# Kernel optimization log

Hardware: AMD Instinct MI355X
Metric: run time of the kernel (lower is better)

Reference implementation:

```python
import jax, jax.numpy as jnp
from jax import lax
import numpy as np

EPS = 1e-5
DN = ('NCHW', 'OIHW', 'NCHW')


def conv_s2(x, w):
    # Conv2d k=4 s=2 p=1, no bias
    return lax.conv_general_dilated(x, w, (2, 2), [(1, 1), (1, 1)], dimension_numbers=DN)


def deconv_s2(x, w):
    # ConvTranspose2d k=4 s=2 p=1; torch weight layout (in, out, kH, kW)
    w_ = jnp.flip(w, (2, 3)).transpose(1, 0, 2, 3)  # -> (out, in, kH, kW)
    return lax.conv_general_dilated(x, w_, (1, 1), [(2, 2), (2, 2)],
                                    lhs_dilation=(2, 2), dimension_numbers=DN)


def bn_train(x, gamma, beta):
    # BatchNorm2d in training mode: batch stats over (N, H, W), biased variance
    m = jnp.mean(x, axis=(0, 2, 3), keepdims=True)
    v = jnp.var(x, axis=(0, 2, 3), keepdims=True)
    g = gamma.reshape(1, -1, 1, 1)
    b = beta.reshape(1, -1, 1, 1)
    return (x - m) * jax.lax.rsqrt(v + EPS) * g + b


def lrelu(x):
    return jnp.where(x >= 0, x, 0.2 * x)


def setup_inputs() -> dict:
    key = jax.random.key(0)
    ks = jax.random.split(key, 32)
    nef = 64
    d = {}
    d['x'] = jax.random.normal(ks[0], (256, 3, 64, 64), dtype=jnp.float32)
    # encoder conv weights (O, I, 4, 4), init N(0, 0.02)
    d['w1'] = 0.02 * jax.random.normal(ks[1], (nef, 3, 4, 4), jnp.float32)
    d['w2'] = 0.02 * jax.random.normal(ks[2], (nef * 2, nef, 4, 4), jnp.float32)
    d['w3'] = 0.02 * jax.random.normal(ks[3], (nef * 4, nef * 2, 4, 4), jnp.float32)
    d['w4'] = 0.02 * jax.random.normal(ks[4], (nef * 8, nef * 4, 4, 4), jnp.float32)
    # bn params: weight ~ N(1, 0.02), bias = 0
    for i, c in enumerate([nef, nef * 2, nef * 4, nef * 8]):
        d[f'g{i+1}'] = 1.0 + 0.02 * jax.random.normal(ks[5 + i], (c,), jnp.float32)
        d[f'b{i+1}'] = jnp.zeros((c,), jnp.float32)
    # 512 channel-wise Linear(16,16): torch default init U(-1/4, 1/4)
    bound = 1.0 / 4.0
    d['cw_w'] = jax.random.uniform(ks[9], (512, 16, 16), jnp.float32, -bound, bound)
    d['cw_b'] = jax.random.uniform(ks[10], (512, 16), jnp.float32, -bound, bound)
    # decoder deconv weights in torch layout (in, out, 4, 4)
    d['dw1'] = 0.02 * jax.random.normal(ks[11], (nef * 8, nef * 4, 4, 4), jnp.float32)
    d['dw2'] = 0.02 * jax.random.normal(ks[12], (nef * 4, nef * 2, 4, 4), jnp.float32)
    d['dw3'] = 0.02 * jax.random.normal(ks[13], (nef * 2, nef, 4, 4), jnp.float32)
    d['dw4'] = 0.02 * jax.random.normal(ks[14], (nef, 3, 4, 4), jnp.float32)
    for i, c in enumerate([nef * 4, nef * 2, nef]):
        d[f'dg{i+1}'] = 1.0 + 0.02 * jax.random.normal(ks[15 + i], (c,), jnp.float32)
        d[f'db{i+1}'] = jnp.zeros((c,), jnp.float32)
    return d


def reference(x, w1, w2, w3, w4, g1, b1, g2, b2, g3, b3, g4, b4,
              cw_w, cw_b, dw1, dw2, dw3, dw4, dg1, db1, dg2, db2, dg3, db3):
    h = lrelu(bn_train(conv_s2(x, w1), g1, b1))
    h = lrelu(bn_train(conv_s2(h, w2), g2, b2))
    h = lrelu(bn_train(conv_s2(h, w3), g3, b3))
    h = lrelu(bn_train(conv_s2(h, w4), g4, b4))  # (B, 512, 4, 4)
    B, C, H, W = h.shape
    flat = h.reshape(B, C, H * W)  # (B, 512, 16)
    # per-channel Linear: y[b,c,t] = sum_s flat[b,c,s] * cw_w[c,t,s] + cw_b[c,t]
    flat = jnp.einsum('bcs,cts->bct', flat, cw_w) + cw_b[None, :, :]
    h = flat.reshape(B, C, H, W)
    h = jax.nn.relu(bn_train(deconv_s2(h, dw1), dg1, db1))
    h = jax.nn.relu(bn_train(deconv_s2(h, dw2), dg2, db2))
    h = jax.nn.relu(bn_train(deconv_s2(h, dw3), dg3, db3))
    return jnp.tanh(deconv_s2(h, dw4))
```

## Files before the change

kernel.cpp:

```cpp
#include <hip/hip_runtime.h>
#include <math.h>

typedef _Float16 f16;
typedef __attribute__((ext_vector_type(8))) _Float16 f16x8;
typedef __attribute__((ext_vector_type(16))) float f32x16;

union U64x2 { unsigned long long u[2]; f16x8 v; };
union Q16   { uint4 q; unsigned long long u[2]; };

constexpr int ilog2c(int x) { return x <= 1 ? 0 : 1 + ilog2c(x >> 1); }

__device__ __forceinline__ float fast_tanh(float x) {
    float e = __expf(2.f * x);
    return (e - 1.f) / (e + 1.f);
}

__device__ __forceinline__ void barrier_no_vmdrain() {
    asm volatile("s_waitcnt lgkmcnt(0)" ::: "memory");
    __builtin_amdgcn_sched_barrier(0);
    __builtin_amdgcn_s_barrier();
    __builtin_amdgcn_sched_barrier(0);
}

template<int CIN,int IH,int IW,int OH,int OW,int COUT,int COB,int SPT,int KS,
         int CO_FR,bool DEC,bool PAIR>
__global__ __launch_bounds__(256,2) void mfma_conv(
    const f16* __restrict__ xin, const f16* __restrict__ wp,
    f16* __restrict__ out16, float* __restrict__ out32, size_t ps,
    float* __restrict__ psumF, float* __restrict__ psqF)
{
    constexpr int OHo  = DEC ? OH/2 : OH;
    constexpr int OWo  = DEC ? OW/2 : OW;
    constexpr int KTOT = CIN * (DEC ? 4 : 16);
    constexpr int CH   = (KTOT/64) / KS;
    constexpr int RPT  = CIN / 64;
    constexpr int RSH  = (RPT==1?0:RPT==2?1:RPT==4?2:3);
    constexpr int WSTR = CIN * 16;
    constexpr int TPR  = 256 / COB;
    constexpr int SPB  = OHo * OWo;
    constexpr int LSPB = ilog2c(SPB);
    constexpr int LOWo = ilog2c(OWo);

    static_assert(!PAIR || (RPT >= 2 && CH % 2 == 0), "PAIR needs RPT>=2");
    constexpr int CHU  = PAIR ? CH/2 : CH;
    constexpr int RW   = PAIR ? 32 : 16;
    constexpr int PM   = PAIR ? 15 : 7;
    constexpr int KKN  = PAIR ? 8 : 4;
    constexpr int XU4  = PAIR ? 16 : 8;
    constexpr int WSEG = (PAIR ? 128 : 64)/TPR;
    constexpr int WU4  = WSEG / 8;

    __shared__ unsigned long long Xs[SPT*RW];
    __shared__ unsigned long long Wls[COB*RW];

    const int t   = threadIdx.x;
    const int bx  = blockIdx.x;
    const int cob = blockIdx.y;
    const int bz  = blockIdx.z;
    const int par = DEC ? (bz & 3) : 0;
    const int ks  = DEC ? (bz >> 2) : bz;
    const int poh = par >> 1, pw = par & 1;

    const int gsp_s = bx*SPT + t;
    const int img_s = gsp_s >> LSPB;
    const int r_s   = gsp_s & (SPB-1);
    const int oy_s  = r_s >> LOWo;
    const int ox_s  = r_s & (OWo-1);

    const int wco   = t / TPR;
    const int wpart = t % TPR;
    const f16* wbase = wp + (size_t)(cob*COB + wco)*WSTR + wpart*WSEG;

    const int wave = t >> 6, lane = t & 63, half = lane >> 5, l31 = lane & 31;
    const int co_w = (wave >> 1) * (CO_FR*32);
    const int sp_w = (wave & 1) * 128;
    const int swz  = l31 & PM;

    f32x16 acc[CO_FR][4];
    #pragma unroll
    for (int i = 0; i < CO_FR; ++i)
        #pragma unroll
        for (int b = 0; b < 4; ++b)
            #pragma unroll
            for (int r = 0; r < 16; ++r) acc[i][b][r] = 0.f;

    uint4 xreg[XU4];
    uint4 wreg[WU4];

    auto issue = [&](int cc) {
        const int gc  = ks*CH + (PAIR ? 2*cc : cc);
        const int tap = gc >> RSH;
        const int ci0 = (gc & (RPT-1)) << 6;
        int kh, kw, ih, iw;
        if (DEC) {
            const int t2h = tap >> 1, t2w = tap & 1;
            kh = (1-poh) + 2*t2h; kw = (1-pw) + 2*t2w;
            ih = oy_s + poh - t2h; iw = ox_s + pw - t2w;
        } else {
            kh = tap >> 2; kw = tap & 3;
            ih = 2*oy_s - 1 + kh; iw = 2*ox_s - 1 + kw;
        }
        const int woff = (kh*4 + kw)*CIN + ci0;
        const uint4* wsrc = (const uint4*)(wbase + woff);
        #pragma unroll
        for (int j = 0; j < WU4; ++j) wreg[j] = wsrc[j];
        const bool ok = (unsigned)ih < (unsigned)IH && (unsigned)iw < (unsigned)IW;
        if (ok) {
            const uint4* xsrc = (const uint4*)
                (xin + ((size_t)(img_s*IH + ih)*IW + iw)*CIN + ci0);
            #pragma unroll
            for (int j = 0; j < XU4; ++j) xreg[j] = xsrc[j];
        } else {
            #pragma unroll
            for (int j = 0; j < XU4; ++j) xreg[j] = uint4{0u,0u,0u,0u};
        }
    };

    issue(0);

    for (int cc = 0; cc < CHU; ++cc) {
        if (cc) barrier_no_vmdrain();

        #pragma unroll
        for (int j = 0; j < WU4; ++j) {
            Q16 v; v.q = wreg[j];
            const int lp = wpart*WU4 + j;
            const int u0 = wco*RW + ((lp ^ (wco & PM)) << 1);
            Wls[u0]   = v.u[0];
            Wls[u0+1] = v.u[1];
        }
        {
            #pragma unroll
            for (int j = 0; j < XU4; ++j) {
                Q16 v; v.q = xreg[j];
                const int u0 = t*RW + ((j ^ (t & PM)) << 1);
                Xs[u0]   = v.u[0];
                Xs[u0+1] = v.u[1];
            }
        }

        if (cc + 1 < CHU) issue(cc + 1);

        asm volatile("s_waitcnt lgkmcnt(0)" ::: "memory");
        __builtin_amdgcn_sched_barrier(0);
        __builtin_amdgcn_s_barrier();
        __builtin_amdgcn_sched_barrier(0);

        #pragma unroll
        for (int kk = 0; kk < KKN; ++kk) {
            const int so = ((kk*2 + half) ^ swz) << 1;
            f16x8 wf[CO_FR], xf[4];
            #pragma unroll
            for (int i = 0; i < CO_FR; ++i) {
                U64x2 u; const int rw = (co_w + i*32 + l31)*RW + so;
                u.u[0] = Wls[rw]; u.u[1] = Wls[rw+1]; wf[i] = u.v;
            }
            #pragma unroll
            for (int b = 0; b < 4; ++b) {
                U64x2 u; const int rx = (sp_w + b*32 + l31)*RW + so;
                u.u[0] = Xs[rx]; u.u[1] = Xs[rx+1]; xf[b] = u.v;
            }
            #pragma unroll
            for (int i = 0; i < CO_FR; ++i)
                #pragma unroll
                for (int b = 0; b < 4; ++b)
                    acc[i][b] = __builtin_amdgcn_mfma_f32_32x32x16_f16(
                        xf[b], wf[i], acc[i][b], 0, 0, 0);
        }
    }

    #pragma unroll
    for (int b = 0; b < 4; ++b) {
        #pragma unroll
        for (int q = 0; q < 4; ++q) {
            #pragma unroll
            for (int r2 = 0; r2 < 4; ++r2) {
                const int sp_loc = sp_w + b*32 + q*8 + 4*half + r2;
                const int gsp    = bx*SPT + sp_loc;
                size_t base;
                if (DEC) {
                    const int img = gsp >> LSPB;
                    const int r   = gsp & (SPB-1);
                    const int oh  = 2*(r >> LOWo) + poh;
                    const int ow  = 2*(r & (OWo-1)) + pw;
                    base = ((size_t)(img*OH + oh)*OW + ow)*COUT + cob*COB;
                } else {
                    base = (size_t)gsp*COUT + cob*COB;
                }
                #pragma unroll
                for (int i = 0; i < CO_FR; ++i) {
                    const int co_l = co_w + i*32 + l31;
                    const float v  = acc[i][b][q*4 + r2];
                    if (KS == 1) out16[base + co_l] = (_Float16)v;
                    else         out32[(size_t)ks*ps + base + co_l] = v;
                }
            }
        }
    }

    if (KS == 1 && psumF != nullptr) {
        float sArr[CO_FR], qArr[CO_FR];
        #pragma unroll
        for (int i = 0; i < CO_FR; ++i) {
            float s = 0.f, q = 0.f;
            #pragma unroll
            for (int b = 0; b < 4; ++b)
                #pragma unroll
                for (int r = 0; r < 16; ++r) {
                    const float v = acc[i][b][r];
                    s += v; q += v * v;
                }
            s += __shfl_down(s, 32);
            q += __shfl_down(q, 32);
            sArr[i] = s; qArr[i] = q;
        }
        __syncthreads();
        float* LS = (float*)Xs;
        float* LQ = LS + 4*CO_FR*32;
        if (half == 0) {
            #pragma unroll
            for (int i = 0; i < CO_FR; ++i) {
                LS[(wave*CO_FR + i)*32 + l31] = sArr[i];
                LQ[(wave*CO_FR + i)*32 + l31] = qArr[i];
            }
        }
        __syncthreads();
        if (t < COB) {
            constexpr int KSH = (CO_FR == 1 ? 5 : 6);
            const int k  = t >> KSH;
            const int ii = (CO_FR == 1) ? 0 : ((t >> 5) & 1);
            const int l  = t & 31;
            const int i0 = ((2*k)  *CO_FR + ii)*32 + l;
            const int i1 = ((2*k+1)*CO_FR + ii)*32 + l;
            atomicAdd(psumF + cob*COB + t, LS[i0] + LS[i1]);
            atomicAdd(psqF  + cob*COB + t, LQ[i0] + LQ[i1]);
        }
    }
}

__global__ __launch_bounds__(256,2) void conv1_mfma(
    const f16* __restrict__ xp, const f16* __restrict__ wp,
    f16* __restrict__ out, float* __restrict__ psumF, float* __restrict__ psqF)
{
    __shared__ unsigned long long Xs[256*16];
    __shared__ unsigned long long Wls[64*16];
    const int t = threadIdx.x, bx = blockIdx.x;

    {
        const int r = t >> 2, part = t & 3;
        const uint4* src = (const uint4*)(wp + r*64 + part*16);
        Q16 v0; v0.q = src[0];
        Q16 v1; v1.q = src[1];
        const int a0 = r*16 + (((part*2)   ^ (r & 7)) << 1);
        const int a1 = r*16 + (((part*2+1) ^ (r & 7)) << 1);
        Wls[a0]   = v0.u[0]; Wls[a0+1] = v0.u[1];
        Wls[a1]   = v1.u[0]; Wls[a1+1] = v1.u[1];
    }
    {
        const int gsp = bx*256 + t;
        const int n = gsp >> 10, r = gsp & 1023;
        const int oy = r >> 5, ox = r & 31;
        const int ih0 = 2*oy - 1, iw0 = 2*ox - 1;
        #pragma unroll
        for (int tap = 0; tap < 16; ++tap) {
            const int ih = ih0 + (tap >> 2), iw = iw0 + (tap & 3);
            unsigned long long v = 0ull;
            if ((unsigned)ih < 64u && (unsigned)iw < 64u)
                v = *(const unsigned long long*)(xp + (((size_t)n*64 + ih)*64 + iw)*4);
            const int u = t*16 + (((tap >> 1) ^ (t & 7)) << 1) + (tap & 1);
            Xs[u] = v;
        }
    }
    __syncthreads();

    const int wave = t >> 6, lane = t & 63, half = lane >> 5, l31 = lane & 31;
    const int co_w = (wave >> 1) * 32;
    const int sp_w = (wave & 1) * 128;
    const int swz  = l31 & 7;

    f32x16 acc[4];
    #pragma unroll
    for (int b = 0; b < 4; ++b)
        #pragma unroll
        for (int r = 0; r < 16; ++r) acc[b][r] = 0.f;

    #pragma unroll
    for (int kk = 0; kk < 4; ++kk) {
        const int so = ((kk*2 + half) ^ swz) << 1;
        U64x2 uw; const int rw = (co_w + l31)*16 + so;
        uw.u[0] = Wls[rw]; uw.u[1] = Wls[rw+1];
        #pragma unroll
        for (int b = 0; b < 4; ++b) {
            U64x2 ux; const int rx = (sp_w + b*32 + l31)*16 + so;
            ux.u[0] = Xs[rx]; ux.u[1] = Xs[rx+1];
            acc[b] = __builtin_amdgcn_mfma_f32_32x32x16_f16(
                ux.v, uw.v, acc[b], 0, 0, 0);
        }
    }
    #pragma unroll
    for (int b = 0; b < 4; ++b)
        #pragma unroll
        for (int q = 0; q < 4; ++q)
            #pragma unroll
            for (int r2 = 0; r2 < 4; ++r2) {
                const int sp_loc = sp_w + b*32 + q*8 + 4*half + r2;
                out[(size_t)(bx*256 + sp_loc)*64 + co_w + l31] =
                    (_Float16)acc[b][q*4 + r2];
            }

    float s = 0.f, q = 0.f;
    #pragma unroll
    for (int b = 0; b < 4; ++b)
        #pragma unroll
        for (int r = 0; r < 16; ++r) {
            const float v = acc[b][r];
            s += v; q += v * v;
        }
    s += __shfl_down(s, 32);
    q += __shfl_down(q, 32);
    __syncthreads();
    {
        float* LS = (float*)Xs;
        float* LQ = LS + 128;
        if (half == 0) {
            LS[wave*32 + l31] = s;
            LQ[wave*32 + l31] = q;
        }
        __syncthreads();
        if (t < 64) {
            const int k = t >> 5, l = t & 31;
            atomicAdd(psumF + t, LS[(2*k)*32 + l] + LS[(2*k+1)*32 + l]);
            atomicAdd(psqF  + t, LQ[(2*k)*32 + l] + LQ[(2*k+1)*32 + l]);
        }
    }
}

__global__ __launch_bounds__(256,2) void deconv3_pwf(
    const f16* __restrict__ xin, const f16* __restrict__ wp,
    f16* __restrict__ out, float* __restrict__ psumF, float* __restrict__ psqF)
{
    __shared__ unsigned long long Xs[256*16];
    __shared__ unsigned long long Wls[2][64*16];

    const int t   = threadIdx.x;
    const int bx  = blockIdx.x;
    const int poh = blockIdx.y;

    const int gsp_s = bx*256 + t;
    const int img_s = gsp_s >> 8;
    const int r_s   = gsp_s & 255;
    const int oy_s  = r_s >> 4;
    const int ox_s  = r_s & 15;

    const int wco   = t >> 2;
    const int wpart = t & 3;
    const f16* wbase = wp + (size_t)wco*2048 + wpart*16;

    const int wave = t >> 6, lane = t & 63, half = lane >> 5, l31 = lane & 31;
    const int co_w = (wave >> 1) * 32;
    const int sp_w = (wave & 1) * 128;
    const int swz  = l31 & 7;

    f32x16 acc[2][4];
    #pragma unroll
    for (int p = 0; p < 2; ++p)
        #pragma unroll
        for (int b = 0; b < 4; ++b)
            #pragma unroll
            for (int r = 0; r < 16; ++r) acc[p][b][r] = 0.f;

    uint4 xreg[8];
    uint4 wregP[2][2];

    auto issue = [&](int cc) {
        const int seg  = cc & 1;
        const int rest = cc >> 1;
        const int dwi  = rest % 3;
        const int t2h  = rest / 3;
        const int dh = poh - t2h, dw = dwi - 1;
        const int ih = oy_s + dh, iw = ox_s + dw;
        const int ci0 = seg << 6;
        #pragma unroll
        for (int p = 0; p < 2; ++p) {
            const int t2w = p - dw;
            if (t2w == 0 || t2w == 1) {
                const int kh = (1-poh) + 2*t2h, kw = (1-p) + 2*t2w;
                const uint4* wsrc = (const uint4*)(wbase + (kh*4 + kw)*128 + ci0);
                wregP[p][0] = wsrc[0];
                wregP[p][1] = wsrc[1];
            }
        }
        const bool ok = (unsigned)ih < 16u && (unsigned)iw < 16u;
        if (ok) {
            const uint4* xsrc = (const uint4*)
                (xin + ((size_t)(img_s*16 + ih)*16 + iw)*128 + ci0);
            #pragma unroll
            for (int j = 0; j < 8; ++j) xreg[j] = xsrc[j];
        } else {
            #pragma unroll
            for (int j = 0; j < 8; ++j) xreg[j] = uint4{0u,0u,0u,0u};
        }
    };

    issue(0);

    for (int cc = 0; cc < 12; ++cc) {
        const int rest = cc >> 1;
        const int dw   = rest % 3 - 1;

        if (cc) barrier_no_vmdrain();

        #pragma unroll
        for (int p = 0; p < 2; ++p) {
            const int t2w = p - dw;
            if (t2w == 0 || t2w == 1) {
                #pragma unroll
                for (int j = 0; j < 2; ++j) {
                    Q16 v; v.q = wregP[p][j];
                    const int lp = wpart*2 + j;
                    const int u0 = wco*16 + ((lp ^ (wco & 7)) << 1);
                    Wls[p][u0]   = v.u[0];
                    Wls[p][u0+1] = v.u[1];
                }
            }
        }
        #pragma unroll
        for (int j = 0; j < 8; ++j) {
            Q16 v; v.q = xreg[j];
            const int u0 = t*16 + ((j ^ (t & 7)) << 1);
            Xs[u0]   = v.u[0];
            Xs[u0+1] = v.u[1];
        }

        if (cc + 1 < 12) issue(cc + 1);

        asm volatile("s_waitcnt lgkmcnt(0)" ::: "memory");
        __builtin_amdgcn_sched_barrier(0);
        __builtin_amdgcn_s_barrier();
        __builtin_amdgcn_sched_barrier(0);

        #pragma unroll
        for (int kk = 0; kk < 4; ++kk) {
            const int so = ((kk*2 + half) ^ swz) << 1;
            f16x8 xf[4];
            #pragma unroll
            for (int b = 0; b < 4; ++b) {
                U64x2 u; const int rx = (sp_w + b*32 + l31)*16 + so;
                u.u[0] = Xs[rx]; u.u[1] = Xs[rx+1]; xf[b] = u.v;
            }
            #pragma unroll
            for (int p = 0; p < 2; ++p) {
                const int t2w = p - dw;
                if (t2w == 0 || t2w == 1) {
                    U64x2 uw; const int rw = (co_w + l31)*16 + so;
                    uw.u[0] = Wls[p][rw]; uw.u[1] = Wls[p][rw+1];
                    #pragma unroll
                    for (int b = 0; b < 4; ++b)
                        acc[p][b] = __builtin_amdgcn_mfma_f32_32x32x16_f16(
                            xf[b], uw.v, acc[p][b], 0, 0, 0);
                }
            }
        }
    }

    #pragma unroll
    for (int p = 0; p < 2; ++p) {
        #pragma unroll
        for (int b = 0; b < 4; ++b) {
            #pragma unroll
            for (int q = 0; q < 4; ++q) {
                #pragma unroll
                for (int r2 = 0; r2 < 4; ++r2) {
                    const int sp_loc = sp_w + b*32 + q*8 + 4*half + r2;
                    const int gsp    = bx*256 + sp_loc;
                    const int img    = gsp >> 8;
                    const int r      = gsp & 255;
                    const int oh     = 2*(r >> 4) + poh;
                    const int ow     = 2*(r & 15) + p;
                    const size_t base = ((size_t)(img*32 + oh)*32 + ow)*64;
                    out[base + co_w + l31] = (_Float16)acc[p][b][q*4 + r2];
                }
            }
        }
    }

    if (psumF != nullptr) {
        float s = 0.f, q = 0.f;
        #pragma unroll
        for (int p = 0; p < 2; ++p)
            #pragma unroll
            for (int b = 0; b < 4; ++b)
                #pragma unroll
                for (int r = 0; r < 16; ++r) {
                    const float v = acc[p][b][r];
                    s += v; q += v * v;
                }
        s += __shfl_down(s, 32);
        q += __shfl_down(q, 32);
        __syncthreads();
        float* LS = (float*)Xs;
        float* LQ = LS + 128;
        if (half == 0) {
            LS[wave*32 + l31] = s;
            LQ[wave*32 + l31] = q;
        }
        __syncthreads();
        if (t < 64) {
            const int k = t >> 5, l = t & 31;
            atomicAdd(psumF + t, LS[(2*k)*32 + l] + LS[(2*k+1)*32 + l]);
            atomicAdd(psqF  + t, LQ[(2*k)*32 + l] + LQ[(2*k+1)*32 + l]);
        }
    }
}

__global__ __launch_bounds__(256,2) void deconv4_mfma(
    const f16* __restrict__ xin, const f16* __restrict__ wp,
    float* __restrict__ out)
{
    __shared__ unsigned long long Xs[256*16];
    __shared__ unsigned long long Wls[4][32*16];

    const int t   = threadIdx.x;
    const int bx  = blockIdx.x;

    const int gsp_s = bx*256 + t;
    const int img_s = gsp_s >> 10;
    const int r_s   = gsp_s & 1023;
    const int oy_s  = r_s >> 5;
    const int ox_s  = r_s & 31;

    const int wco   = t >> 3;
    const int wpart = t & 7;

    const int wave = t >> 6, lane = t & 63, half = lane >> 5, l31 = lane & 31;
    const int sp_w = wave * 64;
    const int swz  = l31 & 7;

    f32x16 acc[4][2];
    #pragma unroll
    for (int p = 0; p < 4; ++p)
        #pragma unroll
        for (int b = 0; b < 2; ++b)
            #pragma unroll
            for (int r = 0; r < 16; ++r) acc[p][b][r] = 0.f;

    uint4 xreg[8];

    auto issueX = [&](int oid) {
        const int dh = oid/3 - 1, dw = oid%3 - 1;
        const int ih = oy_s + dh, iw = ox_s + dw;
        const bool ok = (unsigned)ih < 32u && (unsigned)iw < 32u;
        if (ok) {
            const uint4* src = (const uint4*)
                (xin + ((size_t)(img_s*32 + ih)*32 + iw)*64);
            #pragma unroll
            for (int j = 0; j < 8; ++j) xreg[j] = src[j];
        } else {
            #pragma unroll
            for (int j = 0; j < 8; ++j) xreg[j] = uint4{0u,0u,0u,0u};
        }
    };

    issueX(0);

    #pragma unroll
    for (int oid = 0; oid < 9; ++oid) {
        const int dh = oid/3 - 1, dw = oid%3 - 1;
        const int nH = (dh == 0) ? 2 : 1;
        const int nW = (dw == 0) ? 2 : 1;

        if (oid) barrier_no_vmdrain();

        uint4 wregc[4];
        #pragma unroll
        for (int ch = 0; ch < 2; ++ch) {
            #pragma unroll
            for (int cw = 0; cw < 2; ++cw) {
                if (ch < nH && cw < nW) {
                    const int poh_ = (dh == -1) ? 0 : (dh == 1) ? 1 : ch;
                    const int pw_  = (dw == -1) ? 0 : (dw == 1) ? 1 : cw;
                    const int kh   = (1 - poh_) + 2*(poh_ - dh);
                    const int kw   = (1 - pw_)  + 2*(pw_  - dw);
                    wregc[ch*2+cw] = *(const uint4*)
                        (wp + wco*1024 + (kh*4 + kw)*64 + wpart*8);
                }
            }
        }

        #pragma unroll
        for (int j = 0; j < 8; ++j) {
            Q16 v; v.q = xreg[j];
            const int u0 = t*16 + ((j ^ (t & 7)) << 1);
            Xs[u0]   = v.u[0];
            Xs[u0+1] = v.u[1];
        }
        #pragma unroll
        for (int ch = 0; ch < 2; ++ch) {
            #pragma unroll
            for (int cw = 0; cw < 2; ++cw) {
                if (ch < nH && cw < nW) {
                    Q16 v; v.q = wregc[ch*2+cw];
                    const int u0 = wco*16 + ((wpart ^ (wco & 7)) << 1);
                    Wls[ch*2+cw][u0]   = v.u[0];
                    Wls[ch*2+cw][u0+1] = v.u[1];
                }
            }
        }

        if (oid + 1 < 9) issueX(oid + 1);

        asm volatile("s_waitcnt lgkmcnt(0)" ::: "memory");
        __builtin_amdgcn_sched_barrier(0);
        __builtin_amdgcn_s_barrier();
        __builtin_amdgcn_sched_barrier(0);

        #pragma unroll
        for (int ch = 0; ch < 2; ++ch) {
            #pragma unroll
            for (int cw = 0; cw < 2; ++cw) {
                if (ch < nH && cw < nW) {
                    const int poh_ = (dh == -1) ? 0 : (dh == 1) ? 1 : ch;
                    const int pw_  = (dw == -1) ? 0 : (dw == 1) ? 1 : cw;
                    const int p    = poh_*2 + pw_;
                    #pragma unroll
                    for (int kk = 0; kk < 4; ++kk) {
                        const int so = ((kk*2 + half) ^ swz) << 1;
                        U64x2 uw; const int rw = l31*16 + so;
                        uw.u[0] = Wls[ch*2+cw][rw];
                        uw.u[1] = Wls[ch*2+cw][rw+1];
                        #pragma unroll
                        for (int b = 0; b < 2; ++b) {
                            U64x2 ux; const int rx = (sp_w + b*32 + l31)*16 + so;
                            ux.u[0] = Xs[rx]; ux.u[1] = Xs[rx+1];
                            acc[p][b] = __builtin_amdgcn_mfma_f32_32x32x16_f16(
                                uw.v, ux.v, acc[p][b], 0, 0, 0);
                        }
                    }
                }
            }
        }
    }

    if (half == 0) {
        #pragma unroll
        for (int p = 0; p < 4; ++p) {
            const int poh = p >> 1, pw = p & 1;
            #pragma unroll
            for (int b = 0; b < 2; ++b) {
                const int gsp = bx*256 + sp_w + b*32 + l31;
                const int img = gsp >> 10;
                const int r   = gsp & 1023;
                const int oh  = 2*(r >> 5) + poh;
                const int ow  = 2*(r & 31) + pw;
                #pragma unroll
                for (int co = 0; co < 3; ++co)
                    out[(((size_t)img*3 + co)*64 + oh)*64 + ow] =
                        fast_tanh(acc[p][b][co]);
            }
        }
    }
}

__global__ __launch_bounds__(256) void prep_x(
    const float* __restrict__ x, f16* __restrict__ xp)
{
    const int i = blockIdx.x*256 + threadIdx.x;
    const int n = i >> 12, p = i & 4095;
    const float* b = x + (size_t)n*12288 + p;
    union { _Float16 h[4]; unsigned long long u; } o;
    o.h[0] = (_Float16)b[0];
    o.h[1] = (_Float16)b[4096];
    o.h[2] = (_Float16)b[8192];
    o.h[3] = (_Float16)0.f;
    *(unsigned long long*)(xp + (size_t)i*4) = o.u;
}

__global__ __launch_bounds__(256) void prep_w1(
    const float* __restrict__ w1, f16* __restrict__ wp)
{
    const int e = blockIdx.x*256 + threadIdx.x;
    const int co = e >> 6, k = e & 63, tap = k >> 2, ci = k & 3;
    const float v = (ci < 3) ? w1[(co*3 + ci)*16 + tap] : 0.f;
    wp[e] = (_Float16)v;
}

__global__ __launch_bounds__(256) void prep_w4(
    const float* __restrict__ dw4, f16* __restrict__ wp)
{
    const int e = blockIdx.x*256 + threadIdx.x;
    const int co = e >> 10, r = e & 1023, khw = r >> 6, ci = r & 63;
    const float v = (co < 3) ? dw4[(ci*3 + co)*16 + khw] : 0.f;
    wp[e] = (_Float16)v;
}

__global__ __launch_bounds__(256) void prep_w(
    const float* __restrict__ w2, const float* __restrict__ w3,
    const float* __restrict__ w4, const float* __restrict__ dw1,
    const float* __restrict__ dw2, const float* __restrict__ dw3,
    f16* __restrict__ dst)
{
    const int e = blockIdx.x*256 + threadIdx.x;
    float v;
    if (e < 131072) {
        int co = e >> 10, r = e & 1023, khw = r >> 6, ci = r & 63;
        v = w2[(co*64 + ci)*16 + khw];
    } else if (e < 655360) {
        int l = e - 131072;
        int co = l >> 11, r = l & 2047, khw = r >> 7, ci = r & 127;
        v = w3[(co*128 + ci)*16 + khw];
    } else if (e < 2752512) {
        int l = e - 655360;
        int co = l >> 12, r = l & 4095, khw = r >> 8, ci = r & 255;
        v = w4[(co*256 + ci)*16 + khw];
    } else if (e < 4849664) {
        int l = e - 2752512;
        int co = l >> 13, r = l & 8191, khw = r >> 9, ci = r & 511;
        v = dw1[(ci*256 + co)*16 + khw];
    } else if (e < 5373952) {
        int l = e - 4849664;
        int co = l >> 12, r = l & 4095, khw = r >> 8, ci = r & 255;
        v = dw2[(ci*128 + co)*16 + khw];
    } else {
        int l = e - 5373952;
        int co = l >> 11, r = l & 2047, khw = r >> 7, ci = r & 127;
        v = dw3[(ci*64 + co)*16 + khw];
    }
    dst[e] = (_Float16)v;
}

template<typename T, int P>
__global__ __launch_bounds__(256) void bn_partial(
    const T* __restrict__ x, size_t ps, float* __restrict__ psum,
    float* __restrict__ psq, int C, int rowsPerS, int S)
{
    const int s = blockIdx.x;
    const int c = (blockIdx.y << 6) + (threadIdx.x & 63);
    float a = 0.f, q = 0.f;
    const int rEnd = (s + 1) * rowsPerS;
    for (int r = s*rowsPerS + (threadIdx.x >> 6); r < rEnd; r += 4) {
        float v = 0.f;
        #pragma unroll
        for (int p = 0; p < P; ++p)
            v += (float)x[p*ps + (size_t)r * C + c];
        a += v; q += v * v;
    }
    __shared__ float ls[256], lq[256];
    ls[threadIdx.x] = a; lq[threadIdx.x] = q;
    __syncthreads();
    if (threadIdx.x < 64) {
        a = ls[threadIdx.x] + ls[threadIdx.x+64] + ls[threadIdx.x+128] + ls[threadIdx.x+192];
        q = lq[threadIdx.x] + lq[threadIdx.x+64] + lq[threadIdx.x+128] + lq[threadIdx.x+192];
        psum[c * S + s] = a; psq[c * S + s] = q;
    }
}

__global__ __launch_bounds__(256) void bn_finalize(
    const float* __restrict__ psum, const float* __restrict__ psq,
    const float* __restrict__ gamma, const float* __restrict__ beta,
    float* __restrict__ scale, float* __restrict__ shift,
    int C, int S, float inv_count)
{
    int c = blockIdx.x * 256 + threadIdx.x;
    if (c >= C) return;
    float s = 0.f, q = 0.f;
    for (int i = 0; i < S; ++i) { s += psum[c*S + i]; q += psq[c*S + i]; }
    float m   = s * inv_count;
    float var = q * inv_count - m * m;
    var = var < 0.f ? 0.f : var;
    float sc = gamma[c] * rsqrtf(var + 1e-5f);
    scale[c] = sc;
    shift[c] = beta[c] - m * sc;
}

__global__ __launch_bounds__(256) void bn_act16f(
    f16* __restrict__ x, const float* __restrict__ psum, const float* __restrict__ psq,
    const float* __restrict__ gamma, const float* __restrict__ beta,
    int Cmask, float inv_count, float slope, size_t n8)
{
    const size_t base = (size_t)blockIdx.x*256 + threadIdx.x;
    const int c0 = (int)((base * 8) & (size_t)Cmask);
    float sc[8], sh[8];
    #pragma unroll
    for (int j = 0; j < 8; ++j) {
        const int c = c0 + j;
        float m   = psum[c] * inv_count;
        float var = psq[c] * inv_count - m * m;
        var = var < 0.f ? 0.f : var;
        float s = gamma[c] * rsqrtf(var + 1e-5f);
        sc[j] = s;
        sh[j] = beta[c] - m * s;
    }
    const size_t stride = (size_t)gridDim.x * 256;
    for (size_t i = base; i < n8; i += stride) {
        union { uint4 u; _Float16 h[8]; } a;
        a.u = *(const uint4*)(x + i*8);
        #pragma unroll
        for (int j = 0; j < 8; ++j) {
            float v = (float)a.h[j] * sc[j] + sh[j];
            a.h[j] = (_Float16)(v >= 0.f ? v : slope * v);
        }
        *(uint4*)(x + i*8) = a.u;
    }
}

template<int P>
__global__ __launch_bounds__(256) void bn_act32(
    const float* __restrict__ x, size_t ps, f16* __restrict__ y,
    const float* __restrict__ sc, const float* __restrict__ sh,
    int Cmask, float slope)
{
    const size_t i8 = ((size_t)blockIdx.x*256 + threadIdx.x) * 8;
    float xv[8] = {0,0,0,0,0,0,0,0};
    #pragma unroll
    for (int p = 0; p < P; ++p) {
        float4 v0 = *(const float4*)(x + p*ps + i8);
        float4 v1 = *(const float4*)(x + p*ps + i8 + 4);
        xv[0]+=v0.x; xv[1]+=v0.y; xv[2]+=v0.z; xv[3]+=v0.w;
        xv[4]+=v1.x; xv[5]+=v1.y; xv[6]+=v1.z; xv[7]+=v1.w;
    }
    union { uint4 u; _Float16 h[8]; } a;
    const int c0 = (int)(i8 & (size_t)Cmask);
    #pragma unroll
    for (int j = 0; j < 8; ++j) {
        float v = xv[j] * sc[c0+j] + sh[c0+j];
        a.h[j] = (_Float16)(v >= 0.f ? v : slope * v);
    }
    *(uint4*)(y + i8) = a.u;
}

__global__ __launch_bounds__(256) void chanlin16(
    const f16* __restrict__ in, const float* __restrict__ w,
    const float* __restrict__ bias, f16* __restrict__ out)
{
    const int i = blockIdx.x*256 + threadIdx.x;
    const int c  = i & 511;
    const int bt = i >> 9;
    const int b  = bt >> 4, tt = bt & 15;
    const f16* src = in + ((size_t)b*16)*512 + c;
    const float* wr = w + ((size_t)c*16 + tt)*16;
    float acc = bias[c*16 + tt];
    #pragma unroll
    for (int s = 0; s < 16; ++s)
        acc = fmaf((float)src[s*512], wr[s], acc);
    out[i] = (_Float16)acc;
}

extern "C" void kernel_launch(void* const* d_in, const int* in_sizes, int n_in,
                              void* d_out, int out_size, void* d_ws, size_t ws_size,
                              hipStream_t stream)
{
    const float* x   = (const float*)d_in[0];
    const float* w1  = (const float*)d_in[1];
    const float* w2  = (const float*)d_in[2];
    const float* w3  = (const float*)d_in[3];
    const float* w4  = (const float*)d_in[4];
    const float* g1  = (const float*)d_in[5];
    const float* b1  = (const float*)d_in[6];
    const float* g2  = (const float*)d_in[7];
    const float* b2  = (const float*)d_in[8];
    const float* g3  = (const float*)d_in[9];
    const float* b3  = (const float*)d_in[10];
    const float* g4  = (const float*)d_in[11];
    const float* b4  = (const float*)d_in[12];
    const float* cww = (const float*)d_in[13];
    const float* cwb = (const float*)d_in[14];
    const float* dw1 = (const float*)d_in[15];
    const float* dw2 = (const float*)d_in[16];
    const float* dw3 = (const float*)d_in[17];
    const float* dw4 = (const float*)d_in[18];
    const float* dg1 = (const float*)d_in[19];
    const float* db1 = (const float*)d_in[20];
    const float* dg2 = (const float*)d_in[21];
    const float* db2 = (const float*)d_in[22];
    const float* dg3 = (const float*)d_in[23];
    const float* db3 = (const float*)d_in[24];

    char* WS = (char*)d_ws;
    float* psum  = (float*)WS;
    float* psq   = (float*)(WS + 65536);
    float* scale = (float*)(WS + 131072);
    float* shift = (float*)(WS + 133120);
    float* fst   = (float*)(WS + 196608);
    f16* slotA   = (f16*)(WS + 262144);
    f16* slotB   = (f16*)(WS + 262144 + 33554432);
    f16* wprep   = (f16*)(WS + 84148224);
    f16* wprep1  = wprep + 5505024;
    f16* wprep4  = wprep1 + 4096;

    f16*   A_hi  = slotA + 8388608;
    float* pB    = (float*)slotB;
    f16*   xpack = slotA;

    float* fs0 = fst;          float* fs1 = fst + 1024;
    float* fs2 = fst + 2048;   float* fs4 = fst + 4096;
    float* fs5 = fst + 5120;   float* fs6 = fst + 6144;

    hipMemsetAsync(fst, 0, 28672, stream);
    prep_w<<<21504, 256, 0, stream>>>(w2, w3, w4, dw1, dw2, dw3, wprep);
    prep_w1<<<16, 256, 0, stream>>>(w1, wprep1);
    prep_w4<<<128, 256, 0, stream>>>(dw4, wprep4);
    prep_x<<<4096, 256, 0, stream>>>(x, xpack);

    conv1_mfma<<<1024, 256, 0, stream>>>(xpack, wprep1, slotB, fs0, fs0 + 512);
    bn_act16f<<<2048, 256, 0, stream>>>(slotB, fs0, fs0 + 512, g1, b1, 63,
                                        1.f/262144.f, 0.2f, (size_t)2097152);

    mfma_conv<64,32,32,16,16,128, 128,256,1,2,false,false><<<dim3(256,1,1), 256, 0, stream>>>(
        slotB, wprep, slotA, nullptr, 0, fs1, fs1 + 512);
    bn_act16f<<<2048, 256, 0, stream>>>(slotA, fs1, fs1 + 512, g2, b2, 127,
                                        1.f/65536.f, 0.2f, (size_t)1048576);

    mfma_conv<128,16,16,8,8,256, 64,256,1,1,false,false><<<dim3(64,4,1), 256, 0, stream>>>(
        slotA, wprep + 131072, A_hi, nullptr, 0, fs2, fs2 + 512);
    bn_act16f<<<2048, 256, 0, stream>>>(A_hi, fs2, fs2 + 512, g3, b3, 255,
                                        1.f/16384.f, 0.2f, (size_t)524288);

    mfma_conv<256,8,8,4,4,512, 128,256,4,2,false,false><<<dim3(16,4,4), 256, 0, stream>>>(
        A_hi, wprep + 655360, nullptr, pB, (size_t)2097152, nullptr, nullptr);
    bn_partial<float,4><<<dim3(32,8), 256, 0, stream>>>(pB, (size_t)2097152, psum, psq, 512, 128, 32);
    bn_finalize<<<2, 256, 0, stream>>>(psum, psq, g4, b4, scale, shift, 512, 32, 1.f/4096.f);
    bn_act32<4><<<1024, 256, 0, stream>>>(pB, (size_t)2097152, slotA, scale, shift, 511, 0.2f);

    chanlin16<<<8192, 256, 0, stream>>>(slotA, cww, cwb, slotB);

    mfma_conv<512,4,4,8,8,256, 64,256,1,1,true,false><<<dim3(16,4,4), 256, 0, stream>>>(
        slotB, wprep + 2752512, A_hi, nullptr, 0, fs4, fs4 + 512);
    bn_act16f<<<2048, 256, 0, stream>>>(A_hi, fs4, fs4 + 512, dg1, db1, 255,
                                        1.f/16384.f, 0.f, (size_t)524288);

    mfma_conv<256,8,8,16,16,128, 128,256,1,2,true,false><<<dim3(64,1,4), 256, 0, stream>>>(
        A_hi, wprep + 4849664, slotB, nullptr, 0, fs5, fs5 + 512);
    bn_act16f<<<2048, 256, 0, stream>>>(slotB, fs5, fs5 + 512, dg2, db2, 127,
                                        1.f/65536.f, 0.f, (size_t)1048576);

    deconv3_pwf<<<dim3(256,2), 256, 0, stream>>>(
        slotB, wprep + 5373952, slotA, fs6, fs6 + 512);
    bn_act16f<<<2048, 256, 0, stream>>>(slotA, fs6, fs6 + 512, dg3, db3, 63,
                                        1.f/262144.f, 0.f, (size_t)2097152);

    deconv4_mfma<<<1024, 256, 0, stream>>>(slotA, wprep4, (float*)d_out);
}
```

Measured before the change: 526.6 us.

## Stage haloed input rows once per vertical offset in final deconv

The final transposed-conv kernel used to reload the input tile into shared memory for each of the 9 (dh,dw) neighbour offsets. It now stages a row tile with a one-column halo (34 columns per row) once per vertical offset and reads horizontal shifts by offsetting the LDS column index. That cuts the phases from 9 to 3, with fewer barriers and fewer global loads. In exchange it uses more LDS (8 weight buffers plus a larger X buffer), which may limit occupancy, and it adds irregular halo-fill code run by a subset of threads.

```diff
diff --git a/kernel.cpp b/kernel.cpp
--- a/kernel.cpp
+++ b/kernel.cpp
@@ -513,28 +513,113 @@
     }
 }
 
+static constexpr int D4P0[4] = {0,0,1,1};
+static constexpr int D4KH0[4]= {3,3,3,3};
+static constexpr int D4KW0[4]= {3,1,2,0};
+static constexpr int D4DW0[4]= {-1,0,0,1};
+static constexpr int D4P1[8] = {0,0,1,1,2,2,3,3};
+static constexpr int D4KH1[8]= {1,1,1,1,2,2,2,2};
+static constexpr int D4KW1[8]= {3,1,2,0,3,1,2,0};
+static constexpr int D4DW1[8]= {-1,0,0,1,-1,0,0,1};
+static constexpr int D4P2[4] = {2,2,3,3};
+static constexpr int D4KH2[4]= {0,0,0,0};
+static constexpr int D4KW2[4]= {3,1,2,0};
+static constexpr int D4DW2[4]= {-1,0,0,1};
+
+#define D4_PHASE(DH, PA, KHA, KWA, DWA, NC, LEAD, HASNEXT, NEXTDH)           \
+    {                                                                        \
+        if (LEAD) barrier_no_vmdrain();                                      \
+        uint4 wregc[NC];                                                     \
+        _Pragma("unroll")                                                    \
+        for (int i = 0; i < NC; ++i)                                         \
+            wregc[i] = *(const uint4*)                                       \
+                (wp + wco*1024 + (KHA[i]*4 + KWA[i])*64 + wpart*8);          \
+        {                                                                    \
+            const int c7 = colA & 7;                                         \
+            _Pragma("unroll")                                                \
+            for (int j = 0; j < 8; ++j) {                                    \
+                Q16 v; v.q = xreg[j];                                        \
+                const int u0 = t*16 + ((j ^ c7) << 1);                       \
+                Xs[u0] = v.u[0]; Xs[u0+1] = v.u[1];                          \
+            }                                                                \
+        }                                                                    \
+        if ((t & 15) == 0) {                                                 \
+            const int u2 = 256 + (t >> 4);                                   \
+            const int col2 = u2 - 238;               \
+            const int iy = R0 + (DH) + 7, ix = col2 - 1;                     \
+            const int c7 = col2 & 7;                                         \
+            const bool ok = (unsigned)iy < 32u && (unsigned)ix < 32u;        \
+            if (ok) {                                                        \
+                const uint4* s = (const uint4*)                              \
+                    (xin + ((size_t)(img*32 + iy)*32 + ix)*64);              \
+                _Pragma("unroll")                                            \
+                for (int j = 0; j < 8; ++j) {                                \
+                    Q16 v; v.q = s[j];                                       \
+                    const int u0 = u2*16 + ((j ^ c7) << 1);                  \
+                    Xs[u0] = v.u[0]; Xs[u0+1] = v.u[1];                      \
+                }                                                            \
+            } else {                                                         \
+                _Pragma("unroll")                                            \
+                for (int j = 0; j < 8; ++j) {                                \
+                    const int u0 = u2*16 + ((j ^ c7) << 1);                  \
+                    Xs[u0] = 0ull; Xs[u0+1] = 0ull;                          \
+                }                                                            \
+            }                                                                \
+        }                                                                    \
+        _Pragma("unroll")                                                    \
+        for (int i = 0; i < NC; ++i) {                                       \
+            Q16 v; v.q = wregc[i];                                           \
+            const int u0 = wco*16 + ((wpart ^ (wco & 7)) << 1);              \
+            Wls[i][u0] = v.u[0]; Wls[i][u0+1] = v.u[1];                      \
+        }                                                                    \
+        if (HASNEXT) issueX(NEXTDH);                                         \
+        asm volatile("s_waitcnt lgkmcnt(0)" ::: "memory");                   \
+        __builtin_amdgcn_sched_barrier(0);                                   \
+        __builtin_amdgcn_s_barrier();                                        \
+        __builtin_amdgcn_sched_barrier(0);                                   \
+        _Pragma("unroll")                                                    \
+        for (int i = 0; i < NC; ++i) {                                       \
+            const int dwv = DWA[i], p = PA[i];                               \
+            const int colx = l31 + dwv + 1;                                  \
+            const int cx7  = colx & 7;                                       \
+            _Pragma("unroll")                                                \
+            for (int kk = 0; kk < 4; ++kk) {                                 \
+                const int sw = ((kk*2 + half) ^ (l31 & 7)) << 1;             \
+                const int sx = ((kk*2 + half) ^ cx7) << 1;                   \
+                U64x2 uw; const int rwi = l31*16 + sw;                       \
+                uw.u[0] = Wls[i][rwi]; uw.u[1] = Wls[i][rwi+1];              \
+                _Pragma("unroll")                                            \
+                for (int b = 0; b < 2; ++b) {                                \
+                    const int unit = (wave*2 + b)*34 + colx;                 \
+                    U64x2 ux; const int rx = unit*16 + sx;                   \
+                    ux.u[0] = Xs[rx]; ux.u[1] = Xs[rx+1];                    \
+                    acc[p][b] = __builtin_amdgcn_mfma_f32_32x32x16_f16(      \
+                        uw.v, ux.v, acc[p][b], 0, 0, 0);                     \
+                }                                                            \
+            }                                                                \
+        }                                                                    \
+    }
+
 __global__ __launch_bounds__(256,2) void deconv4_mfma(
     const f16* __restrict__ xin, const f16* __restrict__ wp,
     float* __restrict__ out)
 {
-    __shared__ unsigned long long Xs[256*16];
-    __shared__ unsigned long long Wls[4][32*16];
+    __shared__ unsigned long long Xs[272*16];
+    __shared__ unsigned long long Wls[8][32*16];
 
     const int t   = threadIdx.x;
     const int bx  = blockIdx.x;
 
-    const int gsp_s = bx*256 + t;
-    const int img_s = gsp_s >> 10;
-    const int r_s   = gsp_s & 1023;
-    const int oy_s  = r_s >> 5;
-    const int ox_s  = r_s & 31;
+    const int img = (bx*256) >> 10;
+    const int R0  = ((bx*256) & 1023) >> 5;
 
     const int wco   = t >> 3;
     const int wpart = t & 7;
 
     const int wave = t >> 6, lane = t & 63, half = lane >> 5, l31 = lane & 31;
     const int sp_w = wave * 64;
-    const int swz  = l31 & 7;
+
+    const int rowA = t / 34, colA = t % 34;
 
     f32x16 acc[4][2];
     #pragma unroll
@@ -546,100 +631,25 @@
 
     uint4 xreg[8];
 
-    auto issueX = [&](int oid) {
-        const int dh = oid/3 - 1, dw = oid%3 - 1;
-        const int ih = oy_s + dh, iw = ox_s + dw;
-        const bool ok = (unsigned)ih < 32u && (unsigned)iw < 32u;
+    auto issueX = [&](int dh) {
+        const int iy = R0 + dh + rowA, ix = colA - 1;
+        const bool ok = (unsigned)iy < 32u && (unsigned)ix < 32u;
         if (ok) {
-            const uint4* src = (const uint4*)
-                (xin + ((size_t)(img_s*32 + ih)*32 + iw)*64);
-            #pragma unroll
-            for (int j = 0; j < 8; ++j) xreg[j] = src[j];
+            const uint4* s = (const uint4*)
+                (xin + ((size_t)(img*32 + iy)*32 + ix)*64);
+            #pragma unroll
+            for (int j = 0; j < 8; ++j) xreg[j] = s[j];
         } else {
             #pragma unroll
             for (int j = 0; j < 8; ++j) xreg[j] = uint4{0u,0u,0u,0u};
         }
     };
 
-    issueX(0);
-
-    #pragma unroll
-    for (int oid = 0; oid < 9; ++oid) {
-        const int dh = oid/3 - 1, dw = oid%3 - 1;
-        const int nH = (dh == 0) ? 2 : 1;
-        const int nW = (dw == 0) ? 2 : 1;
-
-        if (oid) barrier_no_vmdrain();
-
-        uint4 wregc[4];
-        #pragma unroll
-        for (int ch = 0; ch < 2; ++ch) {
-            #pragma unroll
-            for (int cw = 0; cw < 2; ++cw) {
-                if (ch < nH && cw < nW) {
-                    const int poh_ = (dh == -1) ? 0 : (dh == 1) ? 1 : ch;
-                    const int pw_  = (dw == -1) ? 0 : (dw == 1) ? 1 : cw;
-                    const int kh   = (1 - poh_) + 2*(poh_ - dh);
-                    const int kw   = (1 - pw_)  + 2*(pw_  - dw);
-                    wregc[ch*2+cw] = *(const uint4*)
-                        (wp + wco*1024 + (kh*4 + kw)*64 + wpart*8);
-                }
-            }
-        }
-
-        #pragma unroll
-        for (int j = 0; j < 8; ++j) {
-            Q16 v; v.q = xreg[j];
-            const int u0 = t*16 + ((j ^ (t & 7)) << 1);
-            Xs[u0]   = v.u[0];
-            Xs[u0+1] = v.u[1];
-        }
-        #pragma unroll
-        for (int ch = 0; ch < 2; ++ch) {
-            #pragma unroll
-            for (int cw = 0; cw < 2; ++cw) {
-                if (ch < nH && cw < nW) {
-                    Q16 v; v.q = wregc[ch*2+cw];
-                    const int u0 = wco*16 + ((wpart ^ (wco & 7)) << 1);
-                    Wls[ch*2+cw][u0]   = v.u[0];
-                    Wls[ch*2+cw][u0+1] = v.u[1];
-                }
-            }
-        }
-
-        if (oid + 1 < 9) issueX(oid + 1);
-
-        asm volatile("s_waitcnt lgkmcnt(0)" ::: "memory");
-        __builtin_amdgcn_sched_barrier(0);
-        __builtin_amdgcn_s_barrier();
-        __builtin_amdgcn_sched_barrier(0);
-
-        #pragma unroll
-        for (int ch = 0; ch < 2; ++ch) {
-            #pragma unroll
-            for (int cw = 0; cw < 2; ++cw) {
-                if (ch < nH && cw < nW) {
-                    const int poh_ = (dh == -1) ? 0 : (dh == 1) ? 1 : ch;
-                    const int pw_  = (dw == -1) ? 0 : (dw == 1) ? 1 : cw;
-                    const int p    = poh_*2 + pw_;
-                    #pragma unroll
-                    for (int kk = 0; kk < 4; ++kk) {
-                        const int so = ((kk*2 + half) ^ swz) << 1;
-                        U64x2 uw; const int rw = l31*16 + so;
-                        uw.u[0] = Wls[ch*2+cw][rw];
-                        uw.u[1] = Wls[ch*2+cw][rw+1];
-                        #pragma unroll
-                        for (int b = 0; b < 2; ++b) {
-                            U64x2 ux; const int rx = (sp_w + b*32 + l31)*16 + so;
-                            ux.u[0] = Xs[rx]; ux.u[1] = Xs[rx+1];
-                            acc[p][b] = __builtin_amdgcn_mfma_f32_32x32x16_f16(
-                                uw.v, ux.v, acc[p][b], 0, 0, 0);
-                        }
-                    }
-                }
-            }
-        }
-    }
+    issueX(-1);
+
+    D4_PHASE(-1, D4P0, D4KH0, D4KW0, D4DW0, 4, false, true, 0)
+    D4_PHASE( 0, D4P1, D4KH1, D4KW1, D4DW1, 8, true,  true, 1)
+    D4_PHASE( 1, D4P2, D4KH2, D4KW2, D4DW2, 4, true,  false, 0)
 
     if (half == 0) {
         #pragma unroll
@@ -648,13 +658,13 @@
             #pragma unroll
             for (int b = 0; b < 2; ++b) {
                 const int gsp = bx*256 + sp_w + b*32 + l31;
-                const int img = gsp >> 10;
+                const int im  = gsp >> 10;
                 const int r   = gsp & 1023;
                 const int oh  = 2*(r >> 5) + poh;
                 const int ow  = 2*(r & 31) + pw;
                 #pragma unroll
                 for (int co = 0; co < 3; ++co)
-                    out[(((size_t)img*3 + co)*64 + oh)*64 + ow] =
+                    out[(((size_t)im*3 + co)*64 + oh)*64 + ow] =
                         fast_tanh(acc[p][b][co]);
             }
         }
```

Measured after the change: 520.5 us, median of 3. About the same (-1.2%).
